# Performance work log

Hardware: AMD Instinct MI355X
Metric: run time of the kernel (lower is better)

The kernel has to match this reference:

```python
import jax, jax.numpy as jnp
import numpy as np

B, H, W = 2, 192, 192
DIM, HEADS, WS = 192, 6, 16
NT, RD, GS = 128, 20, 128
MLP_HID, TD_F, KS = 384, 48, 5
EPS = 1e-5


def _layernorm(x, g, b):
    m = jnp.mean(x, -1, keepdims=True)
    v = jnp.var(x, -1, keepdims=True)
    return (x - m) / jnp.sqrt(v + EPS) * g + b


def _l2n(x):
    return x / jnp.maximum(jnp.linalg.norm(x, axis=-1, keepdims=True), 1e-12)


def _rpi(ws):
    coords = np.stack(np.meshgrid(np.arange(ws), np.arange(ws), indexing='ij'))
    cf = coords.reshape(2, -1)
    rc = (cf[:, :, None] - cf[:, None, :]).transpose(1, 2, 0)
    rc[..., 0] += ws - 1
    rc[..., 1] += ws - 1
    rc[..., 0] *= 2 * ws - 1
    return rc.sum(-1)  # (ws*ws, ws*ws)


RPI = _rpi(WS)


def _win_attn(qkv, rpb, proj_w, h, w):
    # plain W-MSA (shift_size = 0 -> no mask, no roll)
    b, n, c3 = qkv.shape
    c = c3 // 3
    hd = c // HEADS
    nw = WS * WS
    xw = qkv.reshape(b, h // WS, WS, w // WS, WS, c3).transpose(0, 1, 3, 2, 4, 5).reshape(-1, nw, c3)
    bw = xw.shape[0]
    q, k, v = xw.reshape(bw, nw, 3, HEADS, hd).transpose(2, 0, 3, 1, 4)
    attn = (q * hd ** -0.5) @ k.swapaxes(-2, -1)  # (bw, heads, nw, nw)
    bias = rpb[RPI.reshape(-1)].reshape(nw, nw, HEADS).transpose(2, 0, 1)
    attn = jax.nn.softmax(attn + bias[None])
    out = (attn @ v).swapaxes(1, 2).reshape(bw, nw, c) @ proj_w
    out = out.reshape(b, h // WS, w // WS, WS, WS, c).transpose(0, 1, 3, 2, 4, 5).reshape(b, n, c)
    return out


def _atd_ca(x, td, wq, wk, wv, scale_p):
    q = _l2n(x @ wq)   # (b,n,rd)
    k = _l2n(td @ wk)  # (b,m,rd)
    v = td @ wv        # (b,m,c)
    scale = 1.0 + jnp.clip(scale_p, 0.0, 3.0) * np.log(NT)
    attn = jax.nn.softmax((q @ k.swapaxes(-2, -1)) * scale)  # (b,n,m)
    return attn @ v, attn


def _ac_msa(qkv, tk_id, proj_w):
    b, n, c3 = qkv.shape
    c = c3 // 3
    gs = min(n, GS)
    ng = (n + gs - 1) // gs
    pad = ng * gs - n
    idx = jnp.argsort(tk_id, axis=-1)          # sort tokens by category id
    inv = jnp.argsort(idx, axis=-1)            # inverse permutation
    sq = jnp.take_along_axis(qkv, idx[..., None], axis=1)
    if pad > 0:
        sq = jnp.concatenate([sq, sq[:, n - pad:n][:, ::-1]], axis=1)
    q, k, v = sq.reshape(b, ng, gs, 3, HEADS, c // HEADS).transpose(3, 0, 1, 4, 2, 5)
    attn = jax.nn.softmax((q @ k.swapaxes(-2, -1)) * (c // HEADS) ** -0.5)
    out = (attn @ v).transpose(0, 1, 3, 2, 4).reshape(b, ng * gs, c)[:, :n]
    out = jnp.take_along_axis(out, inv[..., None], axis=1)
    return out @ proj_w


def _convffn(x, x_td, w1, dw, w2, h, w):
    y = jnp.concatenate([jax.nn.gelu(x @ w1, approximate=False), x_td], axis=-1)
    b, n, ch = y.shape
    img = y.swapaxes(1, 2).reshape(b, ch, h, w)
    p = (KS - 1) // 2
    conv = jax.lax.conv_general_dilated(img, dw, (1, 1), [(p, p), (p, p)],
                                        dimension_numbers=('NCHW', 'OIHW', 'NCHW'),
                                        feature_group_count=ch)
    conv = jax.nn.gelu(conv, approximate=False).reshape(b, ch, n).swapaxes(1, 2)
    return (y + conv) @ w2


def setup_inputs():
    key = jax.random.key(0)
    ks = jax.random.split(key, 16)
    p = lambda k, s: jax.random.normal(k, s, jnp.float32) * 0.02
    return {
        'x': jax.random.normal(ks[0], (B, H * W, DIM), jnp.float32),
        'td': jax.random.normal(ks[1], (B, NT, DIM), jnp.float32),
        'norm1_g': jnp.ones((DIM,), jnp.float32), 'norm1_b': jnp.zeros((DIM,), jnp.float32),
        'norm2_g': jnp.ones((DIM,), jnp.float32), 'norm2_b': jnp.zeros((DIM,), jnp.float32),
        'wqkv': p(ks[2], (DIM, 3 * DIM)),
        'rpb': p(ks[3], ((2 * WS - 1) ** 2, HEADS)),
        'win_proj': p(ks[4], (DIM, DIM)),
        'atd_wq': p(ks[5], (DIM, RD)),
        'atd_wk': p(ks[6], (DIM, RD)),
        'atd_wv': p(ks[7], (DIM, DIM)),
        'atd_scale': jnp.ones((1,), jnp.float32),
        'aca_proj': p(ks[8], (DIM, DIM)),
        'fc_td_w': p(ks[9], (DIM, TD_F)),
        'ffn_w1': p(ks[10], (DIM, MLP_HID)),
        'ffn_dw': p(ks[11], (MLP_HID + TD_F, 1, KS, KS)),
        'ffn_w2': p(ks[12], (MLP_HID + TD_F, DIM)),
        'h': H, 'w': W,
    }


def reference(x, td, norm1_g, norm1_b, norm2_g, norm2_b, wqkv, rpb, win_proj,
              atd_wq, atd_wk, atd_wv, atd_scale, aca_proj, fc_td_w,
              ffn_w1, ffn_dw, ffn_w2, h, w):
    shortcut = x
    xn = _layernorm(x, norm1_g, norm1_b)
    qkv = xn @ wqkv  # (b, n, 3c)
    x_atd, sim = _atd_ca(xn, td, atd_wq, atd_wk, atd_wv, atd_scale)
    x_aca = _ac_msa(qkv, jnp.argmax(sim, axis=-1), aca_proj)
    x_win = _win_attn(qkv, rpb, win_proj, h, w)
    x = shortcut + x_win + x_atd + x_aca
    x_td = sim @ (td @ fc_td_w)  # (b, n, td_f): dictionary features routed by cross-attn weights
    x = x + _convffn(_layernorm(x, norm2_g, norm2_b), x_td, ffn_w1, ffn_dw, ffn_w2, h, w)
    return x
```

## Files before the change

kernel.cpp:

```cpp
#include <hip/hip_runtime.h>
#include <hip/hip_bf16.h>
#include <math.h>

#define NTOK 36864
#define NTOT 73728
#define CDIM 192
#define C3   576
#define NH   6
#define HD   32
#define RD   20
#define NTD  128
#define GSZ  128
#define NGRP 288
#define MLP  384
#define TDF  48
#define CH   432
#define RAWLD 384
#define TDO_LD 260

typedef __hip_bfloat16 bf16;
typedef __attribute__((ext_vector_type(8))) short short8;
typedef __attribute__((ext_vector_type(4))) float f32x4;

__device__ __forceinline__ float gelu_f(float x) {
    float u = x * (1.5957691216f + 0.0713548162f * x * x);
    return x / (1.0f + __expf(-u));
}

__device__ __forceinline__ unsigned short f32_to_bf16u(float f) {
    unsigned int u = __float_as_uint(f);
    u = (u + 0x7FFFu + ((u >> 16) & 1u)) >> 16;
    return (unsigned short)u;
}

__device__ __forceinline__ unsigned pack2bf(float a, float b) {
    return (__float_as_uint(a) >> 16) | (__float_as_uint(b) & 0xFFFF0000u);
}

__device__ __forceinline__ float bfbits2f(unsigned short u) {
    return __uint_as_float(((unsigned)u) << 16);
}

#define PACKW_TOT (192*576 + 192*192*2 + 192*384 + 432*192 + 192*16 + 192*TDO_LD)

__global__ void ln1_packw_kernel(
        const float* __restrict__ x, const float* __restrict__ g,
        const float* __restrict__ be, float* __restrict__ outf,
        bf16* __restrict__ outh,
        const float* __restrict__ wqkv, const float* __restrict__ wproj,
        const float* __restrict__ aproj, const float* __restrict__ w1,
        const float* __restrict__ w2,
        const float* __restrict__ awk, const float* __restrict__ awv,
        const float* __restrict__ fcw,
        bf16* __restrict__ wqkvT, bf16* __restrict__ projT,
        bf16* __restrict__ w1T, bf16* __restrict__ w2T,
        float* __restrict__ wcomb) {
    if (blockIdx.x < NTOT / 4) {
        long tok = (long)blockIdx.x * 4 + (threadIdx.x >> 6);
        int lane = threadIdx.x & 63;
        const float* row = x + tok * CDIM;
        float v0 = row[lane], v1 = row[lane + 64], v2 = row[lane + 128];
        float s  = v0 + v1 + v2;
        float ss = v0 * v0 + v1 * v1 + v2 * v2;
        #pragma unroll
        for (int o = 32; o > 0; o >>= 1) {
            s  += __shfl_down(s, o);
            ss += __shfl_down(ss, o);
        }
        s = __shfl(s, 0); ss = __shfl(ss, 0);
        float mean = s * (1.0f / 192.0f);
        float var  = ss * (1.0f / 192.0f) - mean * mean;
        float rstd = rsqrtf(var + 1e-5f);
        float r0 = (v0 - mean) * rstd * g[lane]       + be[lane];
        float r1 = (v1 - mean) * rstd * g[lane + 64]  + be[lane + 64];
        float r2 = (v2 - mean) * rstd * g[lane + 128] + be[lane + 128];
        float* orow = outf + tok * CDIM;
        orow[lane] = r0; orow[lane + 64] = r1; orow[lane + 128] = r2;
        bf16* hrow = outh + tok * CDIM;
        hrow[lane]       = __float2bfloat16(r0);
        hrow[lane + 64]  = __float2bfloat16(r1);
        hrow[lane + 128] = __float2bfloat16(r2);
        return;
    }
    int i = (blockIdx.x - NTOT / 4) * 256 + threadIdx.x;
    const int S0 = 192 * 576, S1 = 192 * 192, S2 = 192 * 192, S3 = 192 * 384,
              S4 = 432 * 192, S5 = 192 * 16, S6 = 192 * TDO_LD;
    if (i < S0) { int k = i / 576, n = i % 576; wqkvT[(long)n * 192 + k] = __float2bfloat16(wqkv[i]); return; }
    i -= S0;
    if (i < S1) { int k = i / 192, n = i % 192; projT[(long)n * 384 + k] = __float2bfloat16(wproj[i]); return; }
    i -= S1;
    if (i < S2) { int k = i / 192, n = i % 192; projT[(long)n * 384 + 192 + k] = __float2bfloat16(aproj[i]); return; }
    i -= S2;
    if (i < S3) { int k = i / 384, n = i % 384; w1T[(long)n * 192 + k] = __float2bfloat16(w1[i]); return; }
    i -= S3;
    if (i < S4) { int k = i / 192, n = i % 192; w2T[(long)n * 448 + k] = __float2bfloat16(w2[i]); return; }
    i -= S4;
    if (i < S5) { int n = i / 16, k = i % 16; w2T[(long)n * 448 + 432 + k] = __float2bfloat16(0.0f); return; }
    i -= S5;
    if (i < S6) {
        int k = i / TDO_LD, n = i % TDO_LD;
        float v;
        if (n < RD)            v = awk[k * RD + n];
        else if (n < RD + 192) v = awv[k * 192 + (n - RD)];
        else                   v = fcw[k * TDF + (n - RD - 192)];
        wcomb[(long)k * TDO_LD + n] = v;
    }
}

__global__ void ln2_kernel(const float* __restrict__ x, const float* __restrict__ g,
                           const float* __restrict__ be, bf16* __restrict__ outh) {
    long tok = (long)blockIdx.x * 4 + (threadIdx.x >> 6);
    int lane = threadIdx.x & 63;
    const float* row = x + tok * CDIM;
    float v0 = row[lane], v1 = row[lane + 64], v2 = row[lane + 128];
    float s  = v0 + v1 + v2;
    float ss = v0 * v0 + v1 * v1 + v2 * v2;
    #pragma unroll
    for (int o = 32; o > 0; o >>= 1) {
        s  += __shfl_down(s, o);
        ss += __shfl_down(ss, o);
    }
    s = __shfl(s, 0); ss = __shfl(ss, 0);
    float mean = s * (1.0f / 192.0f);
    float var  = ss * (1.0f / 192.0f) - mean * mean;
    float rstd = rsqrtf(var + 1e-5f);
    float r0 = (v0 - mean) * rstd * g[lane]       + be[lane];
    float r1 = (v1 - mean) * rstd * g[lane + 64]  + be[lane + 64];
    float r2 = (v2 - mean) * rstd * g[lane + 128] + be[lane + 128];
    bf16* hrow = outh + tok * CDIM;
    hrow[lane]       = __float2bfloat16(r0);
    hrow[lane + 64]  = __float2bfloat16(r1);
    hrow[lane + 128] = __float2bfloat16(r2);
}

#define LDT 72
template<int ACC, int GELU, int BF16OUT, int CHUNK8, int ADDX, int PL8OUT = 0>
__global__ void __launch_bounds__(256) gemm_bt(
        const bf16* __restrict__ A, const bf16* __restrict__ Bt,
        void* __restrict__ Cv, const float* __restrict__ Xadd,
        int M, int N, int K, int lda, int ldbt, int ldc,
        long sA, long sB, long sC) {
    long bz = blockIdx.z;
    A  += bz * sA;
    Bt += bz * sB;
    if (BF16OUT) Cv = (void*)((bf16*)Cv + bz * sC);
    else         Cv = (void*)((float*)Cv + bz * sC);
    if (ADDX) Xadd += bz * sC;

    __shared__ short As[128 * LDT];
    __shared__ short Bs[64 * LDT];
    int tid  = threadIdx.x;
    int lane = tid & 63;
    int w    = tid >> 6;
    int wr = w >> 1, wc = w & 1;
    int row0 = blockIdx.y * 128, col0 = blockIdx.x * 64;
    int fr = lane & 15, fq = lane >> 4;
    f32x4 acc[4][2];
    #pragma unroll
    for (int m = 0; m < 4; ++m)
        #pragma unroll
        for (int n = 0; n < 2; ++n) acc[m][n] = (f32x4)(0.0f);

    int sa_row = tid >> 3;
    int sa_kc  = (tid & 7) * 8;
    int sb_col = tid & 63;
    int sb_kb  = (tid >> 6) * 16;
    bool cok = (col0 + sb_col) < N;

    for (int k0 = 0; k0 < K; k0 += 64) {
        __syncthreads();
        int kk = k0 + sa_kc;
        #pragma unroll
        for (int p = 0; p < 4; ++p) {
            int r = sa_row + p * 32;
            short8 v = (short8)(0);
            if (kk + 8 <= K) {
                const bf16* src;
                if (CHUNK8)
                    src = A + ((long)(kk >> 3) * NTOT + row0 + r) * 8;
                else
                    src = A + (long)(row0 + r) * lda + kk;
                v = *(const short8*)src;
            } else if (!CHUNK8 && kk < K) {
                #pragma unroll
                for (int i = 0; i < 8; ++i)
                    v[i] = (kk + i < K) ? *(const short*)&A[(long)(row0 + r) * lda + kk + i]
                                        : (short)0;
            }
            *(short8*)&As[r * LDT + sa_kc] = v;
        }
        {
            short8 v0 = (short8)(0), v1 = (short8)(0);
            if (cok) {
                const bf16* src = Bt + (long)(col0 + sb_col) * ldbt + k0 + sb_kb;
                v0 = *(const short8*)src;
                v1 = *(const short8*)(src + 8);
            }
            *(short8*)&Bs[sb_col * LDT + sb_kb]     = v0;
            *(short8*)&Bs[sb_col * LDT + sb_kb + 8] = v1;
        }
        __syncthreads();
        short8 af[4][2], bf_[2][2];
        #pragma unroll
        for (int m = 0; m < 4; ++m) {
            int r = wr * 64 + m * 16 + fr;
            af[m][0] = *(const short8*)&As[r * LDT + fq * 8];
            af[m][1] = *(const short8*)&As[r * LDT + 32 + fq * 8];
        }
        #pragma unroll
        for (int n = 0; n < 2; ++n) {
            int c = wc * 32 + n * 16 + fr;
            bf_[n][0] = *(const short8*)&Bs[c * LDT + fq * 8];
            bf_[n][1] = *(const short8*)&Bs[c * LDT + 32 + fq * 8];
        }
        #pragma unroll
        for (int m = 0; m < 4; ++m)
            #pragma unroll
            for (int n = 0; n < 2; ++n) {
                acc[m][n] = __builtin_amdgcn_mfma_f32_16x16x32_bf16(
                                af[m][0], bf_[n][0], acc[m][n], 0, 0, 0);
                acc[m][n] = __builtin_amdgcn_mfma_f32_16x16x32_bf16(
                                af[m][1], bf_[n][1], acc[m][n], 0, 0, 0);
            }
    }
    #pragma unroll
    for (int m = 0; m < 4; ++m) {
        #pragma unroll
        for (int n = 0; n < 2; ++n) {
            int gc = col0 + wc * 32 + n * 16 + fr;
            if (gc >= N) continue;
            #pragma unroll
            for (int r = 0; r < 4; ++r) {
                int gr = row0 + wr * 64 + m * 16 + fq * 4 + r;
                float vv = acc[m][n][r];
                if (GELU) vv = gelu_f(vv);
                if (BF16OUT) {
                    long o;
                    if (PL8OUT) o = ((long)(gc >> 3) * NTOT + gr) * 8 + (gc & 7);
                    else        o = (long)gr * ldc + gc;
                    ((bf16*)Cv)[o] = __float2bfloat16(vv);
                } else {
                    long o = (long)gr * ldc + gc;
                    float* Cc = (float*)Cv;
                    if (ADDX) Cc[o] = Xadd[o] + vv;
                    else if (ACC) Cc[o] += vv;
                    else Cc[o] = vv;
                }
            }
        }
    }
}

template<int ACC, int GELU, int TDPACK>
__global__ void __launch_bounds__(256) gemm_kernel(
        const float* __restrict__ A, const float* __restrict__ B,
        float* __restrict__ Cc, int M, int N, int K, int lda, int ldb, int ldc,
        bf16* __restrict__ vtdT, bf16* __restrict__ tdfT) {
    __shared__ float As[16][68];
    __shared__ float Bs[16][68];
    int tid = threadIdx.x;
    int tr = tid >> 4, tc = tid & 15;
    int row0 = blockIdx.y * 64, col0 = blockIdx.x * 64;
    float acc[4][4] = {};
    int lm = tid >> 4;
    int lk = tid & 15;
    int bk = tid >> 6;
    int bn = tid & 63;
    for (int k0 = 0; k0 < K; k0 += 16) {
        #pragma unroll
        for (int i = 0; i < 4; ++i) {
            int m = lm + i * 16;
            int gr = row0 + m;
            As[lk][m] = (gr < M) ? A[(long)gr * lda + (k0 + lk)] : 0.0f;
        }
        #pragma unroll
        for (int i = 0; i < 4; ++i) {
            int kk = bk + i * 4;
            int gc = col0 + bn;
            Bs[kk][bn] = (gc < N) ? B[(long)(k0 + kk) * ldb + gc] : 0.0f;
        }
        __syncthreads();
        #pragma unroll
        for (int kk = 0; kk < 16; ++kk) {
            float4 av = *(const float4*)&As[kk][tr * 4];
            float4 bv = *(const float4*)&Bs[kk][tc * 4];
            float a[4] = {av.x, av.y, av.z, av.w};
            float b[4] = {bv.x, bv.y, bv.z, bv.w};
            #pragma unroll
            for (int i = 0; i < 4; ++i)
                #pragma unroll
                for (int j = 0; j < 4; ++j)
                    acc[i][j] = fmaf(a[i], b[j], acc[i][j]);
        }
        __syncthreads();
    }
    #pragma unroll
    for (int i = 0; i < 4; ++i) {
        int gr = row0 + tr * 4 + i;
        if (gr >= M) continue;
        #pragma unroll
        for (int j = 0; j < 4; ++j) {
            int gc = col0 + tc * 4 + j;
            if (gc >= N) continue;
            float v = acc[i][j];
            if (GELU) v = gelu_f(v);
            long o = (long)gr * ldc + gc;
            if (ACC) Cc[o] += v; else Cc[o] = v;
            if (TDPACK && gc >= RD) {
                bf16 hv = __float2bfloat16(v);
                int bb = gr >> 7;
                int kk2 = gr & (NTD - 1);
                if (gc < RD + CDIM)
                    vtdT[(long)bb * CDIM * NTD + (long)(gc - RD) * NTD + kk2] = hv;
                else
                    tdfT[(long)bb * TDF * NTD + (long)(gc - RD - CDIM) * NTD + kk2] = hv;
            }
        }
    }
}

__global__ void __launch_bounds__(256) qn_kernel(
        const float* __restrict__ xn, const float* __restrict__ awq,
        float* __restrict__ qn) {
    __shared__ float aw[192 * RD];
    __shared__ float xs[256 * 33];
    int tid = threadIdx.x;
    long tok0 = (long)blockIdx.x * 256;
    for (int e = tid; e < 192 * RD; e += 256) aw[e] = awq[e];
    float acc[RD];
    #pragma unroll
    for (int j = 0; j < RD; ++j) acc[j] = 0.0f;
    for (int kc = 0; kc < 192; kc += 32) {
        __syncthreads();
        for (int e = tid; e < 256 * 32; e += 256) {
            int tk = e >> 5, kk = e & 31;
            xs[tk * 33 + kk] = xn[(tok0 + tk) * CDIM + kc + kk];
        }
        __syncthreads();
        #pragma unroll 8
        for (int kk = 0; kk < 32; ++kk) {
            float v = xs[tid * 33 + kk];
            const float* ar = &aw[(kc + kk) * RD];
            #pragma unroll
            for (int j = 0; j < RD; ++j) acc[j] = fmaf(v, ar[j], acc[j]);
        }
    }
    float ss = 0.0f;
    #pragma unroll
    for (int j = 0; j < RD; ++j) ss += acc[j] * acc[j];
    float inv = 1.0f / fmaxf(sqrtf(ss), 1e-12f);
    float* orow = qn + (tok0 + tid) * RD;
    #pragma unroll
    for (int j = 0; j < RD; ++j) orow[j] = acc[j] * inv;
}

__global__ void __launch_bounds__(256) sim_kernel(
        const float* __restrict__ qn, const float* __restrict__ kn,
        const float* __restrict__ scale_p, bf16* __restrict__ sim,
        int* __restrict__ tkid) {
    int lane = threadIdx.x & 63;
    long tok = (long)blockIdx.x * 4 + (threadIdx.x >> 6);
    int b = (tok >= NTOK) ? 1 : 0;
    float q[RD];
    const float* qrow = qn + tok * RD;
    #pragma unroll
    for (int r = 0; r < RD; ++r) q[r] = qrow[r];
    const float* k0 = kn + ((long)b * NTD + lane) * TDO_LD;
    const float* k1 = k0 + (long)64 * TDO_LD;
    float k0v[RD], k1v[RD];
    #pragma unroll
    for (int r = 0; r < RD; ++r) { k0v[r] = k0[r]; k1v[r] = k1[r]; }
    float ss0 = 0.0f, ss1 = 0.0f;
    #pragma unroll
    for (int r = 0; r < RD; ++r) {
        ss0 += k0v[r] * k0v[r];
        ss1 += k1v[r] * k1v[r];
    }
    float inv0 = 1.0f / fmaxf(sqrtf(ss0), 1e-12f);
    float inv1 = 1.0f / fmaxf(sqrtf(ss1), 1e-12f);
    float s0 = 0.0f, s1 = 0.0f;
    #pragma unroll
    for (int r = 0; r < RD; ++r) {
        s0 = fmaf(q[r], k0v[r] * inv0, s0);
        s1 = fmaf(q[r], k1v[r] * inv1, s1);
    }
    float scl = 1.0f + fminf(fmaxf(scale_p[0], 0.0f), 3.0f) * logf(128.0f);
    s0 *= scl; s1 *= scl;
    float m; int mi;
    if (s0 >= s1) { m = s0; mi = lane; } else { m = s1; mi = lane + 64; }
    #pragma unroll
    for (int o = 1; o < 64; o <<= 1) {
        float om = __shfl_xor(m, o);
        int   oi = __shfl_xor(mi, o);
        if (om > m || (om == m && oi < mi)) { m = om; mi = oi; }
    }
    float p0 = __expf(s0 - m), p1 = __expf(s1 - m);
    float t = p0 + p1;
    #pragma unroll
    for (int o = 1; o < 64; o <<= 1) t += __shfl_xor(t, o);
    float inv = 1.0f / t;
    bf16* srow = sim + tok * NTD;
    srow[lane]      = __float2bfloat16(p0 * inv);
    srow[lane + 64] = __float2bfloat16(p1 * inv);
    if (lane == 0) tkid[tok] = mi;
}

__global__ void hist_kernel(const int* __restrict__ tkid, int* __restrict__ hist) {
    int tile = blockIdx.x;
    int tid = threadIdx.x;
    __shared__ int h[NTD];
    h[tid] = 0;
    __syncthreads();
    atomicAdd(&h[tkid[tile * GSZ + tid]], 1);
    __syncthreads();
    hist[tile * NTD + tid] = h[tid];
}

__global__ void __launch_bounds__(64) scan1_kernel(int* __restrict__ hist,
                                                   int* __restrict__ tot) {
    int bc = blockIdx.x;
    int b = bc >> 7, c = bc & (NTD - 1);
    int lane = threadIdx.x;
    if (lane < 32) {
        int base = (b * NGRP + lane * 9) * NTD + c;
        int v[9];
        int s = 0;
        #pragma unroll
        for (int k = 0; k < 9; ++k) { v[k] = hist[base + k * NTD]; s += v[k]; }
        int run = s;
        #pragma unroll
        for (int o = 1; o < 32; o <<= 1) {
            int t = __shfl_up(run, o);
            if (lane >= o) run += t;
        }
        if (lane == 31) tot[bc] = run;
        int acc = run - s;
        #pragma unroll
        for (int k = 0; k < 9; ++k) { hist[base + k * NTD] = acc; acc += v[k]; }
    }
}

__global__ void __launch_bounds__(128) scatter_kernel(const int* __restrict__ tkid,
                                                      const int* __restrict__ hist,
                                                      const int* __restrict__ tot,
                                                      int* __restrict__ idxs) {
    int tile = blockIdx.x;
    int b = tile / NGRP;
    int gl = tile % NGRP;
    int tid = threadIdx.x;
    __shared__ int cats[GSZ];
    __shared__ int basec[NTD];
    __shared__ int wsum[2];
    {
        int lane = tid & 63, wv = tid >> 6;
        int s = tot[b * NTD + tid];
        int run = s;
        #pragma unroll
        for (int o = 1; o < 64; o <<= 1) {
            int t = __shfl_up(run, o);
            if (lane >= o) run += t;
        }
        if (lane == 63) wsum[wv] = run;
        __syncthreads();
        int add = (wv == 1) ? wsum[0] : 0;
        basec[tid] = run - s + add;
    }
    int cat = tkid[tile * GSZ + tid];
    cats[tid] = cat;
    __syncthreads();
    int rank = 0;
    for (int j = 0; j < tid; ++j) rank += (cats[j] == cat) ? 1 : 0;
    int pos = hist[tile * NTD + cat] + basec[cat] + rank;
    idxs[b * NTOK + pos] = gl * GSZ + tid;
}

#define VLDW 264
#define VLDA 136


__global__ void __launch_bounds__(256) win_mfma(
        const bf16* __restrict__ qkv, const float* __restrict__ rpb,
        bf16* __restrict__ raw) {
    int t2  = blockIdx.x;
    int h   = t2 % NH;
    int wid = t2 / NH;
    int b = wid / 144;
    int wrem = wid % 144;
    int wy = wrem / 12, wx = wrem % 12;
    long base_tok = (long)b * NTOK;

    __shared__ short Kt[256 * 40];
    __shared__ short Vt[32 * VLDW];
    __shared__ float rb[961];

    int tid = threadIdx.x;
    int lane = tid & 63;
    int wv = tid >> 6;
    int fr = lane & 15, fq = lane >> 4;
    const float scl = 0.17677669529663687f;

    for (int i = tid; i < 961; i += 256) rb[i] = rpb[i * NH + h];

    short8 qf[4];
    #pragma unroll
    for (int m = 0; m < 4; ++m) {
        int q = wv * 64 + m * 16 + fr;
        long nq = base_tok + (long)(wy * 16 + (q >> 4)) * 192 + (wx * 16 + (q & 15));
        qf[m] = *(const short8*)(qkv + nq * C3 + h * HD + fq * 8);
    }

    {
        int s_ = tid >> 2, ch = tid & 3;
        #pragma unroll
        for (int t = 0; t < 4; ++t) {
            int p = t * 64 + s_;
            long nk = base_tok + (long)(wy * 16 + (p >> 4)) * 192 + (wx * 16 + (p & 15));
            const bf16* kb = qkv + nk * C3 + CDIM + h * HD + ch * 8;
            *(short8*)&Kt[p * 40 + ch * 8] = *(const short8*)kb;
            short8 vv = *(const short8*)(kb + CDIM);
            #pragma unroll
            for (int i = 0; i < 8; ++i)
                Vt[(ch * 8 + i) * VLDW + p] = vv[i];
        }
    }
    __syncthreads();

    f32x4 acc[4][2];
    float lst[4];
    #pragma unroll
    for (int m = 0; m < 4; ++m) {
        acc[m][0] = (f32x4)(0.0f); acc[m][1] = (f32x4)(0.0f);
        lst[m] = 0.0f;
    }

    for (int t = 0; t < 4; ++t) {
        short8 ak[4], av[2][2];
        #pragma unroll
        for (int c = 0; c < 4; ++c)
            ak[c] = *(const short8*)&Kt[(t * 64 + c * 16 + fr) * 40 + fq * 8];
        #pragma unroll
        for (int n = 0; n < 2; ++n)
            #pragma unroll
            for (int ks = 0; ks < 2; ++ks)
                av[n][ks] = *(const short8*)&Vt[(n * 16 + fr) * VLDW + t * 64 + ks * 32 + fq * 8];

        #pragma unroll
        for (int m = 0; m < 4; ++m) {
            int q = wv * 64 + m * 16 + fr;
            int iy = q >> 4, ix = q & 15;
            int bxb = ix + 15 - 4 * fq;
            float s[4][4];
            #pragma unroll
            for (int c = 0; c < 4; ++c) {
                f32x4 s4 = (f32x4)(0.0f);
                s4 = __builtin_amdgcn_mfma_f32_16x16x32_bf16(ak[c], qf[m], s4, 0, 0, 0);
                const float* rbp = &rb[(iy + 15 - (t * 4 + c)) * 31 + bxb];
                #pragma unroll
                for (int r = 0; r < 4; ++r)
                    s[c][r] = s4[r] * scl + rbp[-r];
            }
            float ps = 0.0f;
            #pragma unroll
            for (int c = 0; c < 4; ++c)
                #pragma unroll
                for (int r = 0; r < 4; ++r) {
                    float p = __expf(s[c][r]);
                    s[c][r] = p;
                    ps += p;
                }
            ps += __shfl_xor(ps, 16);
            ps += __shfl_xor(ps, 32);
            lst[m] += ps;
            unsigned pk[4][2];
            #pragma unroll
            for (int c = 0; c < 4; ++c) {
                pk[c][0] = pack2bf(s[c][0], s[c][1]);
                pk[c][1] = pack2bf(s[c][2], s[c][3]);
            }
            #pragma unroll
            for (int ks = 0; ks < 2; ++ks) {
                unsigned u[4];
                #pragma unroll
                for (int jj = 0; jj < 4; ++jj) {
                    int src = fr + 16 * (2 * (fq & 1) + (jj >> 1));
                    unsigned lo = (unsigned)__shfl((int)pk[2 * ks][jj & 1], src);
                    unsigned hi = (unsigned)__shfl((int)pk[2 * ks + 1][jj & 1], src);
                    u[jj] = (fq & 2) ? hi : lo;
                }
                short8 pb;
                #pragma unroll
                for (int jj = 0; jj < 4; ++jj) {
                    pb[2 * jj]     = (short)(u[jj] & 0xFFFF);
                    pb[2 * jj + 1] = (short)(u[jj] >> 16);
                }
                #pragma unroll
                for (int n = 0; n < 2; ++n)
                    acc[m][n] = __builtin_amdgcn_mfma_f32_16x16x32_bf16(
                                    av[n][ks], pb, acc[m][n], 0, 0, 0);
            }
        }
    }
    #pragma unroll
    for (int m = 0; m < 4; ++m) {
        int q = wv * 64 + m * 16 + fr;
        long nq = base_tok + (long)(wy * 16 + (q >> 4)) * 192 + (wx * 16 + (q & 15));
        float inv = 1.0f / lst[m];
        #pragma unroll
        for (int n = 0; n < 2; ++n) {
            uint2 wv2;
            wv2.x = pack2bf(acc[m][n][0] * inv, acc[m][n][1] * inv);
            wv2.y = pack2bf(acc[m][n][2] * inv, acc[m][n][3] * inv);
            *(uint2*)(raw + nq * RAWLD + h * HD + n * 16 + 4 * fq) = wv2;
        }
    }
}

__global__ void __launch_bounds__(128) aca_mfma(
        const bf16* __restrict__ qkv, const int* __restrict__ idxs,
        bf16* __restrict__ raw) {
    int t2   = blockIdx.x;
    int h    = t2 % NH;
    int grp  = t2 / NH;
    int b = grp / NGRP;
    int g = grp % NGRP;
    long btok = (long)b * NTOK;

    __shared__ short Kt[128 * 40];
    __shared__ short Vt[32 * VLDA];
    __shared__ int   sidx[GSZ];

    int tid = threadIdx.x;
    int lane = tid & 63;
    int half = tid >> 6;
    int fr = lane & 15, fq = lane >> 4;
    const float scl = 0.17677669529663687f;

    sidx[tid] = idxs[btok + g * GSZ + tid];
    __syncthreads();

    short8 qf[4];
    #pragma unroll
    for (int m = 0; m < 4; ++m) {
        long n = btok + sidx[half * 64 + m * 16 + fr];
        qf[m] = *(const short8*)(qkv + n * C3 + h * HD + fq * 8);
    }

    {
        int s_ = tid >> 1, hf = tid & 1;
        int d0 = hf * 16;
        #pragma unroll
        for (int t = 0; t < 2; ++t) {
            int p = t * 64 + s_;
            long n = btok + sidx[p];
            const bf16* kb = qkv + n * C3 + CDIM + h * HD + d0;
            *(short8*)&Kt[p * 40 + d0]     = *(const short8*)kb;
            *(short8*)&Kt[p * 40 + d0 + 8] = *(const short8*)(kb + 8);
            short8 v0 = *(const short8*)(kb + CDIM);
            short8 v1 = *(const short8*)(kb + CDIM + 8);
            #pragma unroll
            for (int i = 0; i < 8; ++i) {
                Vt[(d0 + i) * VLDA + p]     = v0[i];
                Vt[(d0 + 8 + i) * VLDA + p] = v1[i];
            }
        }
    }
    __syncthreads();

    f32x4 acc[4][2];
    float lst[4];
    #pragma unroll
    for (int m = 0; m < 4; ++m) {
        acc[m][0] = (f32x4)(0.0f); acc[m][1] = (f32x4)(0.0f);
        lst[m] = 0.0f;
    }

    for (int t = 0; t < 2; ++t) {
        short8 ak[4], av[2][2];
        #pragma unroll
        for (int c = 0; c < 4; ++c)
            ak[c] = *(const short8*)&Kt[(t * 64 + c * 16 + fr) * 40 + fq * 8];
        #pragma unroll
        for (int n = 0; n < 2; ++n)
            #pragma unroll
            for (int ks = 0; ks < 2; ++ks)
                av[n][ks] = *(const short8*)&Vt[(n * 16 + fr) * VLDA + t * 64 + ks * 32 + fq * 8];

        #pragma unroll
        for (int m = 0; m < 4; ++m) {
            float s[4][4];
            #pragma unroll
            for (int c = 0; c < 4; ++c) {
                f32x4 s4 = (f32x4)(0.0f);
                s4 = __builtin_amdgcn_mfma_f32_16x16x32_bf16(ak[c], qf[m], s4, 0, 0, 0);
                #pragma unroll
                for (int r = 0; r < 4; ++r) s[c][r] = s4[r] * scl;
            }
            float ps = 0.0f;
            #pragma unroll
            for (int c = 0; c < 4; ++c)
                #pragma unroll
                for (int r = 0; r < 4; ++r) {
                    float p = __expf(s[c][r]);
                    s[c][r] = p;
                    ps += p;
                }
            ps += __shfl_xor(ps, 16);
            ps += __shfl_xor(ps, 32);
            lst[m] += ps;
            unsigned pk[4][2];
            #pragma unroll
            for (int c = 0; c < 4; ++c) {
                pk[c][0] = pack2bf(s[c][0], s[c][1]);
                pk[c][1] = pack2bf(s[c][2], s[c][3]);
            }
            #pragma unroll
            for (int ks = 0; ks < 2; ++ks) {
                unsigned u[4];
                #pragma unroll
                for (int jj = 0; jj < 4; ++jj) {
                    int src = fr + 16 * (2 * (fq & 1) + (jj >> 1));
                    unsigned lo = (unsigned)__shfl((int)pk[2 * ks][jj & 1], src);
                    unsigned hi = (unsigned)__shfl((int)pk[2 * ks + 1][jj & 1], src);
                    u[jj] = (fq & 2) ? hi : lo;
                }
                short8 pb;
                #pragma unroll
                for (int jj = 0; jj < 4; ++jj) {
                    pb[2 * jj]     = (short)(u[jj] & 0xFFFF);
                    pb[2 * jj + 1] = (short)(u[jj] >> 16);
                }
                #pragma unroll
                for (int n = 0; n < 2; ++n)
                    acc[m][n] = __builtin_amdgcn_mfma_f32_16x16x32_bf16(
                                    av[n][ks], pb, acc[m][n], 0, 0, 0);
            }
        }
    }
    #pragma unroll
    for (int m = 0; m < 4; ++m) {
        long n = btok + sidx[half * 64 + m * 16 + fr];
        float inv = 1.0f / lst[m];
        #pragma unroll
        for (int nn = 0; nn < 2; ++nn) {
            uint2 wv2;
            wv2.x = pack2bf(acc[m][nn][0] * inv, acc[m][nn][1] * inv);
            wv2.y = pack2bf(acc[m][nn][2] * inv, acc[m][nn][3] * inv);
            *(uint2*)(raw + n * RAWLD + CDIM + h * HD + nn * 16 + 4 * fq) = wv2;
        }
    }
}

#define CPS 1296
__global__ void __launch_bounds__(256) conv_kernel(
        const bf16* __restrict__ y, const float* __restrict__ dw,
        bf16* __restrict__ zc) {
    int bid = blockIdx.x;
    int ck   = bid % 54;
    int tile = (bid / 54) % 36;
    int b    = bid / (54 * 36);
    int ty = tile / 6, tx = tile % 6;
    int c0 = ck * 8;
    __shared__ float ys[8 * CPS];
    __shared__ float wt[8 * 25];
    int tid = threadIdx.x;
    const bf16* ypl = y + ((long)ck * NTOT + (long)b * NTOK) * 8;
    for (int p = tid; p < 1296; p += 256) {
        int ly = p / 36, lx = p - ly * 36;
        int gy = ty * 32 + ly - 2, gx = tx * 32 + lx - 2;
        float f[8];
        if (gy >= 0 && gy < 192 && gx >= 0 && gx < 192) {
            short8 hv = *(const short8*)(ypl + (long)(gy * 192 + gx) * 8);
            #pragma unroll
            for (int i = 0; i < 8; ++i) f[i] = bfbits2f((unsigned short)hv[i]);
        } else {
            #pragma unroll
            for (int i = 0; i < 8; ++i) f[i] = 0.0f;
        }
        #pragma unroll
        for (int i = 0; i < 8; ++i) ys[i * CPS + p] = f[i];
    }
    for (int e = tid; e < 200; e += 256) wt[e] = dw[c0 * 25 + e];
    __syncthreads();
    int col = tid & 31, r4 = tid >> 5;
    int py0 = r4 * 4;
    long tok0 = (long)b * NTOK + (long)(ty * 32 + py0) * 192 + tx * 32 + col;
    unsigned hh[4][4];
    for (int c = 0; c < 8; ++c) {
        const float* yc = &ys[c * CPS];
        float w[25];
        #pragma unroll
        for (int t = 0; t < 25; ++t) w[t] = wt[c * 25 + t];
        float a[4] = {0.0f, 0.0f, 0.0f, 0.0f};
        #pragma unroll
        for (int dy2 = 0; dy2 < 8; ++dy2) {
            float rv[5];
            #pragma unroll
            for (int dx = 0; dx < 5; ++dx)
                rv[dx] = yc[(py0 + dy2) * 36 + col + dx];
            #pragma unroll
            for (int i = 0; i < 4; ++i) {
                int dy = dy2 - i;
                if (dy >= 0 && dy < 5) {
                    #pragma unroll
                    for (int dx = 0; dx < 5; ++dx)
                        a[i] = fmaf(rv[dx], w[dy * 5 + dx], a[i]);
                }
            }
        }
        #pragma unroll
        for (int i = 0; i < 4; ++i) {
            float center = yc[(py0 + i + 2) * 36 + col + 2];
            unsigned short hsh = f32_to_bf16u(center + gelu_f(a[i]));
            if (c & 1) hh[i][c >> 1] |= ((unsigned)hsh) << 16;
            else       hh[i][c >> 1] = (unsigned)hsh;
        }
    }
    #pragma unroll
    for (int i = 0; i < 4; ++i) {
        long tok = tok0 + (long)i * 192;
        *(uint4*)(zc + ((long)ck * NTOT + tok) * 8) =
            make_uint4(hh[i][0], hh[i][1], hh[i][2], hh[i][3]);
    }
}

extern "C" void kernel_launch(void* const* d_in, const int* in_sizes, int n_in,
                              void* d_out, int out_size, void* d_ws, size_t ws_size,
                              hipStream_t stream) {
    (void)in_sizes; (void)n_in; (void)out_size; (void)ws_size;
    const float* x     = (const float*)d_in[0];
    const float* td    = (const float*)d_in[1];
    const float* n1g   = (const float*)d_in[2];
    const float* n1b   = (const float*)d_in[3];
    const float* n2g   = (const float*)d_in[4];
    const float* n2b   = (const float*)d_in[5];
    const float* wqkv  = (const float*)d_in[6];
    const float* rpb   = (const float*)d_in[7];
    const float* wproj = (const float*)d_in[8];
    const float* awq   = (const float*)d_in[9];
    const float* awk   = (const float*)d_in[10];
    const float* awv   = (const float*)d_in[11];
    const float* ascl  = (const float*)d_in[12];
    const float* aproj = (const float*)d_in[13];
    const float* fcw   = (const float*)d_in[14];
    const float* w1    = (const float*)d_in[15];
    const float* dw    = (const float*)d_in[16];
    const float* w2    = (const float*)d_in[17];
    float* out = (float*)d_out;

    char* ws = (char*)d_ws;
    size_t off = 0;
    auto alloc = [&](size_t bytes) -> char* {
        char* p = ws + off;
        off += (bytes + 255) & ~(size_t)255;
        return p;
    };
    bf16*  qkv  = (bf16*)alloc((size_t)NTOT * C3 * 2);
    float* xn   = (float*)alloc((size_t)NTOT * CDIM * 4);
    bf16*  xnh  = (bf16*)alloc((size_t)NTOT * CDIM * 2);
    float* qn   = (float*)alloc((size_t)NTOT * RD * 4);
    bf16*  simb = (bf16*)alloc((size_t)NTOT * NTD * 2);
    float* tdo  = (float*)alloc((size_t)2 * NTD * TDO_LD * 4);
    float* wcomb= (float*)alloc((size_t)192 * TDO_LD * 4);
    bf16*  vtdT = (bf16*)alloc((size_t)2 * CDIM * NTD * 2);
    bf16*  tdfT = (bf16*)alloc((size_t)2 * TDF * NTD * 2);
    bf16*  wqkvT= (bf16*)alloc((size_t)C3 * CDIM * 2);
    bf16*  projT= (bf16*)alloc((size_t)CDIM * 384 * 2);
    bf16*  w1T  = (bf16*)alloc((size_t)MLP * CDIM * 2);
    bf16*  w2T  = (bf16*)alloc((size_t)CDIM * 448 * 2);
    int*   tkid = (int*)alloc((size_t)NTOT * 4);
    int*   idxs = (int*)alloc((size_t)NTOT * 4);
    int*   hist = (int*)alloc((size_t)576 * NTD * 4);
    int*   tot  = (int*)alloc((size_t)2 * NTD * 4);
    bf16*  y    = qkv;
    bf16*  raw  = (bf16*)xn;
    bf16*  zc   = (bf16*)xn;

    ln1_packw_kernel<<<NTOT / 4 + (PACKW_TOT + 255) / 256, 256, 0, stream>>>(
        x, n1g, n1b, xn, xnh,
        wqkv, wproj, aproj, w1, w2, awk, awv, fcw,
        wqkvT, projT, w1T, w2T, wcomb);

    gemm_bt<0,0,1,0,0><<<dim3(9, 576), 256, 0, stream>>>(
        xnh, wqkvT, qkv, nullptr, NTOT, C3, CDIM, CDIM, CDIM, C3, 0, 0, 0);

    qn_kernel<<<NTOT / 256, 256, 0, stream>>>(xn, awq, qn);

    gemm_kernel<0,0,1><<<dim3(5, 4), 256, 0, stream>>>(
        td, wcomb, tdo, 2 * NTD, TDO_LD, CDIM, CDIM, TDO_LD, TDO_LD, vtdT, tdfT);

    sim_kernel<<<NTOT / 4, 256, 0, stream>>>(qn, tdo, ascl, simb, tkid);

    gemm_bt<0,0,0,0,1><<<dim3(3, 288, 2), 256, 0, stream>>>(
        simb, vtdT, out, x, NTOK, CDIM, NTD, NTD, NTD, CDIM,
        (long)NTOK * NTD, (long)CDIM * NTD, (long)NTOK * CDIM);

    hist_kernel<<<576, 128, 0, stream>>>(tkid, hist);
    scan1_kernel<<<2 * NTD, 64, 0, stream>>>(hist, tot);
    scatter_kernel<<<576, 128, 0, stream>>>(tkid, hist, tot, idxs);

    win_mfma<<<288 * NH, 256, 0, stream>>>(qkv, rpb, raw);
    aca_mfma<<<576 * NH, 128, 0, stream>>>(qkv, idxs, raw);
    gemm_bt<1,0,0,0,0><<<dim3(3, 576), 256, 0, stream>>>(
        raw, projT, out, nullptr, NTOT, CDIM, 384, RAWLD, 384, CDIM, 0, 0, 0);

    gemm_bt<0,0,1,0,0,1><<<dim3(1, 288, 2), 256, 0, stream>>>(
        simb, tdfT, y + (long)48 * NTOT * 8, nullptr, NTOK, TDF, NTD, NTD, NTD, 0,
        (long)NTOK * NTD, (long)TDF * NTD, (long)NTOK * 8);

    ln2_kernel<<<NTOT / 4, 256, 0, stream>>>(out, n2g, n2b, xnh);

    gemm_bt<0,1,1,0,0,1><<<dim3(6, 576), 256, 0, stream>>>(
        xnh, w1T, y, nullptr, NTOT, MLP, CDIM, CDIM, CDIM, 0, 0, 0, 0);

    conv_kernel<<<2 * 36 * 54, 256, 0, stream>>>(y, dw, zc);
    gemm_bt<1,0,0,1,0><<<dim3(3, 576), 256, 0, stream>>>(
        zc, w2T, out, nullptr, NTOT, CDIM, CH, 0, 448, CDIM, 0, 0, 0);
}
```

Measured before the change: 663.6 us.

## Fold histogram into sim kernel and merge window and category attention launches

Drops the separate histogram kernel: the LN1/weight-pack kernel now zeroes the histogram buffer, and sim_kernel adds each token's argmax straight into the per-tile histogram with a global atomic. The window-attention and category-attention kernels are merged into one launch that picks its role from the block index, with two 128-thread category subgroups packed per 256-thread block over shared memory. This removes two kernel launches and lets both attention types run at the same time, at the cost of global atomic contention in sim_kernel and a larger shared-memory footprint for the category blocks. The category path still has __syncthreads across both subgroups, which is fine as long as the control flow is uniform.

```diff
diff --git a/kernel.cpp b/kernel.cpp
--- a/kernel.cpp
+++ b/kernel.cpp
@@ -42,6 +42,7 @@
 }
 
 #define PACKW_TOT (192*576 + 192*192*2 + 192*384 + 432*192 + 192*16 + 192*TDO_LD)
+#define HISTZ_TOT (576 * NTD)
 
 __global__ void ln1_packw_kernel(
         const float* __restrict__ x, const float* __restrict__ g,
@@ -54,7 +55,7 @@
         const float* __restrict__ fcw,
         bf16* __restrict__ wqkvT, bf16* __restrict__ projT,
         bf16* __restrict__ w1T, bf16* __restrict__ w2T,
-        float* __restrict__ wcomb) {
+        float* __restrict__ wcomb, int* __restrict__ hist) {
     if (blockIdx.x < NTOT / 4) {
         long tok = (long)blockIdx.x * 4 + (threadIdx.x >> 6);
         int lane = threadIdx.x & 63;
@@ -84,7 +85,7 @@
     }
     int i = (blockIdx.x - NTOT / 4) * 256 + threadIdx.x;
     const int S0 = 192 * 576, S1 = 192 * 192, S2 = 192 * 192, S3 = 192 * 384,
-              S4 = 432 * 192, S5 = 192 * 16, S6 = 192 * TDO_LD;
+              S4 = 432 * 192, S5 = 192 * 16, S6 = 192 * TDO_LD, S7 = HISTZ_TOT;
     if (i < S0) { int k = i / 576, n = i % 576; wqkvT[(long)n * 192 + k] = __float2bfloat16(wqkv[i]); return; }
     i -= S0;
     if (i < S1) { int k = i / 192, n = i % 192; projT[(long)n * 384 + k] = __float2bfloat16(wproj[i]); return; }
@@ -104,7 +105,10 @@
         else if (n < RD + 192) v = awv[k * 192 + (n - RD)];
         else                   v = fcw[k * TDF + (n - RD - 192)];
         wcomb[(long)k * TDO_LD + n] = v;
-    }
+        return;
+    }
+    i -= S6;
+    if (i < S7) hist[i] = 0;
 }
 
 __global__ void ln2_kernel(const float* __restrict__ x, const float* __restrict__ g,
@@ -357,7 +361,7 @@
 __global__ void __launch_bounds__(256) sim_kernel(
         const float* __restrict__ qn, const float* __restrict__ kn,
         const float* __restrict__ scale_p, bf16* __restrict__ sim,
-        int* __restrict__ tkid) {
+        int* __restrict__ tkid, int* __restrict__ hist) {
     int lane = threadIdx.x & 63;
     long tok = (long)blockIdx.x * 4 + (threadIdx.x >> 6);
     int b = (tok >= NTOK) ? 1 : 0;
@@ -402,18 +406,10 @@
     bf16* srow = sim + tok * NTD;
     srow[lane]      = __float2bfloat16(p0 * inv);
     srow[lane + 64] = __float2bfloat16(p1 * inv);
-    if (lane == 0) tkid[tok] = mi;
-}
-
-__global__ void hist_kernel(const int* __restrict__ tkid, int* __restrict__ hist) {
-    int tile = blockIdx.x;
-    int tid = threadIdx.x;
-    __shared__ int h[NTD];
-    h[tid] = 0;
-    __syncthreads();
-    atomicAdd(&h[tkid[tile * GSZ + tid]], 1);
-    __syncthreads();
-    hist[tile * NTD + tid] = h[tid];
+    if (lane == 0) {
+        tkid[tok] = mi;
+        atomicAdd(&hist[(tok >> 7) * NTD + mi], 1);
+    }
 }
 
 __global__ void __launch_bounds__(64) scan1_kernel(int* __restrict__ hist,
@@ -477,165 +473,165 @@
 #define VLDW 264
 #define VLDA 136
 
-
-__global__ void __launch_bounds__(256) win_mfma(
+#define WIN_BLOCKS (288 * NH)
+__global__ void __launch_bounds__(256) attn_mfma(
         const bf16* __restrict__ qkv, const float* __restrict__ rpb,
-        bf16* __restrict__ raw) {
-    int t2  = blockIdx.x;
-    int h   = t2 % NH;
-    int wid = t2 / NH;
-    int b = wid / 144;
-    int wrem = wid % 144;
-    int wy = wrem / 12, wx = wrem % 12;
-    long base_tok = (long)b * NTOK;
-
-    __shared__ short Kt[256 * 40];
-    __shared__ short Vt[32 * VLDW];
-    __shared__ float rb[961];
-
+        const int* __restrict__ idxs, bf16* __restrict__ raw) {
+    __shared__ __align__(16) char smem[41280];
     int tid = threadIdx.x;
-    int lane = tid & 63;
-    int wv = tid >> 6;
-    int fr = lane & 15, fq = lane >> 4;
-    const float scl = 0.17677669529663687f;
-
-    for (int i = tid; i < 961; i += 256) rb[i] = rpb[i * NH + h];
-
-    short8 qf[4];
-    #pragma unroll
-    for (int m = 0; m < 4; ++m) {
-        int q = wv * 64 + m * 16 + fr;
-        long nq = base_tok + (long)(wy * 16 + (q >> 4)) * 192 + (wx * 16 + (q & 15));
-        qf[m] = *(const short8*)(qkv + nq * C3 + h * HD + fq * 8);
-    }
-
-    {
-        int s_ = tid >> 2, ch = tid & 3;
-        #pragma unroll
-        for (int t = 0; t < 4; ++t) {
-            int p = t * 64 + s_;
-            long nk = base_tok + (long)(wy * 16 + (p >> 4)) * 192 + (wx * 16 + (p & 15));
-            const bf16* kb = qkv + nk * C3 + CDIM + h * HD + ch * 8;
-            *(short8*)&Kt[p * 40 + ch * 8] = *(const short8*)kb;
-            short8 vv = *(const short8*)(kb + CDIM);
-            #pragma unroll
-            for (int i = 0; i < 8; ++i)
-                Vt[(ch * 8 + i) * VLDW + p] = vv[i];
-        }
-    }
-    __syncthreads();
-
-    f32x4 acc[4][2];
-    float lst[4];
-    #pragma unroll
-    for (int m = 0; m < 4; ++m) {
-        acc[m][0] = (f32x4)(0.0f); acc[m][1] = (f32x4)(0.0f);
-        lst[m] = 0.0f;
-    }
-
-    for (int t = 0; t < 4; ++t) {
-        short8 ak[4], av[2][2];
-        #pragma unroll
-        for (int c = 0; c < 4; ++c)
-            ak[c] = *(const short8*)&Kt[(t * 64 + c * 16 + fr) * 40 + fq * 8];
-        #pragma unroll
-        for (int n = 0; n < 2; ++n)
-            #pragma unroll
-            for (int ks = 0; ks < 2; ++ks)
-                av[n][ks] = *(const short8*)&Vt[(n * 16 + fr) * VLDW + t * 64 + ks * 32 + fq * 8];
-
+
+    if (blockIdx.x < WIN_BLOCKS) {
+        short* Kt = (short*)smem;
+        short* Vt = (short*)(smem + 20480);
+        float* rb = (float*)(smem + 20480 + 16896);
+        int t2  = blockIdx.x;
+        int h   = t2 % NH;
+        int wid = t2 / NH;
+        int b = wid / 144;
+        int wrem = wid % 144;
+        int wy = wrem / 12, wx = wrem % 12;
+        long base_tok = (long)b * NTOK;
+
+        int lane = tid & 63;
+        int wv = tid >> 6;
+        int fr = lane & 15, fq = lane >> 4;
+        const float scl = 0.17677669529663687f;
+
+        for (int i = tid; i < 961; i += 256) rb[i] = rpb[i * NH + h];
+
+        short8 qf[4];
         #pragma unroll
         for (int m = 0; m < 4; ++m) {
             int q = wv * 64 + m * 16 + fr;
-            int iy = q >> 4, ix = q & 15;
-            int bxb = ix + 15 - 4 * fq;
-            float s[4][4];
-            #pragma unroll
-            for (int c = 0; c < 4; ++c) {
-                f32x4 s4 = (f32x4)(0.0f);
-                s4 = __builtin_amdgcn_mfma_f32_16x16x32_bf16(ak[c], qf[m], s4, 0, 0, 0);
-                const float* rbp = &rb[(iy + 15 - (t * 4 + c)) * 31 + bxb];
-                #pragma unroll
-                for (int r = 0; r < 4; ++r)
-                    s[c][r] = s4[r] * scl + rbp[-r];
-            }
-            float ps = 0.0f;
+            long nq = base_tok + (long)(wy * 16 + (q >> 4)) * 192 + (wx * 16 + (q & 15));
+            qf[m] = *(const short8*)(qkv + nq * C3 + h * HD + fq * 8);
+        }
+
+        {
+            int s_ = tid >> 2, ch = tid & 3;
+            #pragma unroll
+            for (int t = 0; t < 4; ++t) {
+                int p = t * 64 + s_;
+                long nk = base_tok + (long)(wy * 16 + (p >> 4)) * 192 + (wx * 16 + (p & 15));
+                const bf16* kb = qkv + nk * C3 + CDIM + h * HD + ch * 8;
+                *(short8*)&Kt[p * 40 + ch * 8] = *(const short8*)kb;
+                short8 vv = *(const short8*)(kb + CDIM);
+                #pragma unroll
+                for (int i = 0; i < 8; ++i)
+                    Vt[(ch * 8 + i) * VLDW + p] = vv[i];
+            }
+        }
+        __syncthreads();
+
+        f32x4 acc[4][2];
+        float lst[4];
+        #pragma unroll
+        for (int m = 0; m < 4; ++m) {
+            acc[m][0] = (f32x4)(0.0f); acc[m][1] = (f32x4)(0.0f);
+            lst[m] = 0.0f;
+        }
+
+        for (int t = 0; t < 4; ++t) {
+            short8 ak[4], av[2][2];
             #pragma unroll
             for (int c = 0; c < 4; ++c)
-                #pragma unroll
-                for (int r = 0; r < 4; ++r) {
-                    float p = __expf(s[c][r]);
-                    s[c][r] = p;
-                    ps += p;
+                ak[c] = *(const short8*)&Kt[(t * 64 + c * 16 + fr) * 40 + fq * 8];
+            #pragma unroll
+            for (int n = 0; n < 2; ++n)
+                #pragma unroll
+                for (int ks = 0; ks < 2; ++ks)
+                    av[n][ks] = *(const short8*)&Vt[(n * 16 + fr) * VLDW + t * 64 + ks * 32 + fq * 8];
+
+            #pragma unroll
+            for (int m = 0; m < 4; ++m) {
+                int q = wv * 64 + m * 16 + fr;
+                int iy = q >> 4, ix = q & 15;
+                int bxb = ix + 15 - 4 * fq;
+                float s[4][4];
+                #pragma unroll
+                for (int c = 0; c < 4; ++c) {
+                    f32x4 s4 = (f32x4)(0.0f);
+                    s4 = __builtin_amdgcn_mfma_f32_16x16x32_bf16(ak[c], qf[m], s4, 0, 0, 0);
+                    const float* rbp = &rb[(iy + 15 - (t * 4 + c)) * 31 + bxb];
+                    #pragma unroll
+                    for (int r = 0; r < 4; ++r)
+                        s[c][r] = s4[r] * scl + rbp[-r];
                 }
-            ps += __shfl_xor(ps, 16);
-            ps += __shfl_xor(ps, 32);
-            lst[m] += ps;
-            unsigned pk[4][2];
-            #pragma unroll
-            for (int c = 0; c < 4; ++c) {
-                pk[c][0] = pack2bf(s[c][0], s[c][1]);
-                pk[c][1] = pack2bf(s[c][2], s[c][3]);
-            }
-            #pragma unroll
-            for (int ks = 0; ks < 2; ++ks) {
-                unsigned u[4];
-                #pragma unroll
-                for (int jj = 0; jj < 4; ++jj) {
-                    int src = fr + 16 * (2 * (fq & 1) + (jj >> 1));
-                    unsigned lo = (unsigned)__shfl((int)pk[2 * ks][jj & 1], src);
-                    unsigned hi = (unsigned)__shfl((int)pk[2 * ks + 1][jj & 1], src);
-                    u[jj] = (fq & 2) ? hi : lo;
+                float ps = 0.0f;
+                #pragma unroll
+                for (int c = 0; c < 4; ++c)
+                    #pragma unroll
+                    for (int r = 0; r < 4; ++r) {
+                        float p = __expf(s[c][r]);
+                        s[c][r] = p;
+                        ps += p;
+                    }
+                ps += __shfl_xor(ps, 16);
+                ps += __shfl_xor(ps, 32);
+                lst[m] += ps;
+                unsigned pk[4][2];
+                #pragma unroll
+                for (int c = 0; c < 4; ++c) {
+                    pk[c][0] = pack2bf(s[c][0], s[c][1]);
+                    pk[c][1] = pack2bf(s[c][2], s[c][3]);
                 }
-                short8 pb;
-                #pragma unroll
-                for (int jj = 0; jj < 4; ++jj) {
-                    pb[2 * jj]     = (short)(u[jj] & 0xFFFF);
-                    pb[2 * jj + 1] = (short)(u[jj] >> 16);
+                #pragma unroll
+                for (int ks = 0; ks < 2; ++ks) {
+                    unsigned u[4];
+                    #pragma unroll
+                    for (int jj = 0; jj < 4; ++jj) {
+                        int src = fr + 16 * (2 * (fq & 1) + (jj >> 1));
+                        unsigned lo = (unsigned)__shfl((int)pk[2 * ks][jj & 1], src);
+                        unsigned hi = (unsigned)__shfl((int)pk[2 * ks + 1][jj & 1], src);
+                        u[jj] = (fq & 2) ? hi : lo;
+                    }
+                    short8 pb;
+                    #pragma unroll
+                    for (int jj = 0; jj < 4; ++jj) {
+                        pb[2 * jj]     = (short)(u[jj] & 0xFFFF);
+                        pb[2 * jj + 1] = (short)(u[jj] >> 16);
+                    }
+                    #pragma unroll
+                    for (int n = 0; n < 2; ++n)
+                        acc[m][n] = __builtin_amdgcn_mfma_f32_16x16x32_bf16(
+                                        av[n][ks], pb, acc[m][n], 0, 0, 0);
                 }
-                #pragma unroll
-                for (int n = 0; n < 2; ++n)
-                    acc[m][n] = __builtin_amdgcn_mfma_f32_16x16x32_bf16(
-                                    av[n][ks], pb, acc[m][n], 0, 0, 0);
-            }
-        }
-    }
-    #pragma unroll
-    for (int m = 0; m < 4; ++m) {
-        int q = wv * 64 + m * 16 + fr;
-        long nq = base_tok + (long)(wy * 16 + (q >> 4)) * 192 + (wx * 16 + (q & 15));
-        float inv = 1.0f / lst[m];
-        #pragma unroll
-        for (int n = 0; n < 2; ++n) {
-            uint2 wv2;
-            wv2.x = pack2bf(acc[m][n][0] * inv, acc[m][n][1] * inv);
-            wv2.y = pack2bf(acc[m][n][2] * inv, acc[m][n][3] * inv);
-            *(uint2*)(raw + nq * RAWLD + h * HD + n * 16 + 4 * fq) = wv2;
-        }
-    }
-}
-
-__global__ void __launch_bounds__(128) aca_mfma(
-        const bf16* __restrict__ qkv, const int* __restrict__ idxs,
-        bf16* __restrict__ raw) {
-    int t2   = blockIdx.x;
+            }
+        }
+        #pragma unroll
+        for (int m = 0; m < 4; ++m) {
+            int q = wv * 64 + m * 16 + fr;
+            long nq = base_tok + (long)(wy * 16 + (q >> 4)) * 192 + (wx * 16 + (q & 15));
+            float inv = 1.0f / lst[m];
+            #pragma unroll
+            for (int n = 0; n < 2; ++n) {
+                uint2 wv2;
+                wv2.x = pack2bf(acc[m][n][0] * inv, acc[m][n][1] * inv);
+                wv2.y = pack2bf(acc[m][n][2] * inv, acc[m][n][3] * inv);
+                *(uint2*)(raw + nq * RAWLD + h * HD + n * 16 + 4 * fq) = wv2;
+            }
+        }
+        return;
+    }
+
+    int sub  = tid >> 7;
+    int tidl = tid & 127;
+    int t2   = (blockIdx.x - WIN_BLOCKS) * 2 + sub;
+    short* Kt = (short*)(smem + sub * 19456);
+    short* Vt = (short*)(smem + sub * 19456 + 10240);
+    int* sidx = (int*)  (smem + sub * 19456 + 10240 + 8704);
     int h    = t2 % NH;
     int grp  = t2 / NH;
     int b = grp / NGRP;
     int g = grp % NGRP;
     long btok = (long)b * NTOK;
 
-    __shared__ short Kt[128 * 40];
-    __shared__ short Vt[32 * VLDA];
-    __shared__ int   sidx[GSZ];
-
-    int tid = threadIdx.x;
-    int lane = tid & 63;
-    int half = tid >> 6;
+    int lane = tidl & 63;
+    int half = tidl >> 6;
     int fr = lane & 15, fq = lane >> 4;
     const float scl = 0.17677669529663687f;
 
-    sidx[tid] = idxs[btok + g * GSZ + tid];
+    sidx[tidl] = idxs[btok + g * GSZ + tidl];
     __syncthreads();
 
     short8 qf[4];
@@ -646,7 +642,7 @@
     }
 
     {
-        int s_ = tid >> 1, hf = tid & 1;
+        int s_ = tidl >> 1, hf = tidl & 1;
         int d0 = hf * 16;
         #pragma unroll
         for (int t = 0; t < 2; ++t) {
@@ -875,10 +871,10 @@
     bf16*  raw  = (bf16*)xn;
     bf16*  zc   = (bf16*)xn;
 
-    ln1_packw_kernel<<<NTOT / 4 + (PACKW_TOT + 255) / 256, 256, 0, stream>>>(
+    ln1_packw_kernel<<<NTOT / 4 + (PACKW_TOT + HISTZ_TOT + 255) / 256, 256, 0, stream>>>(
         x, n1g, n1b, xn, xnh,
         wqkv, wproj, aproj, w1, w2, awk, awv, fcw,
-        wqkvT, projT, w1T, w2T, wcomb);
+        wqkvT, projT, w1T, w2T, wcomb, hist);
 
     gemm_bt<0,0,1,0,0><<<dim3(9, 576), 256, 0, stream>>>(
         xnh, wqkvT, qkv, nullptr, NTOT, C3, CDIM, CDIM, CDIM, C3, 0, 0, 0);
@@ -888,18 +884,16 @@
     gemm_kernel<0,0,1><<<dim3(5, 4), 256, 0, stream>>>(
         td, wcomb, tdo, 2 * NTD, TDO_LD, CDIM, CDIM, TDO_LD, TDO_LD, vtdT, tdfT);
 
-    sim_kernel<<<NTOT / 4, 256, 0, stream>>>(qn, tdo, ascl, simb, tkid);
+    sim_kernel<<<NTOT / 4, 256, 0, stream>>>(qn, tdo, ascl, simb, tkid, hist);
 
     gemm_bt<0,0,0,0,1><<<dim3(3, 288, 2), 256, 0, stream>>>(
         simb, vtdT, out, x, NTOK, CDIM, NTD, NTD, NTD, CDIM,
         (long)NTOK * NTD, (long)CDIM * NTD, (long)NTOK * CDIM);
 
-    hist_kernel<<<576, 128, 0, stream>>>(tkid, hist);
     scan1_kernel<<<2 * NTD, 64, 0, stream>>>(hist, tot);
     scatter_kernel<<<576, 128, 0, stream>>>(tkid, hist, tot, idxs);
 
-    win_mfma<<<288 * NH, 256, 0, stream>>>(qkv, rpb, raw);
-    aca_mfma<<<576 * NH, 128, 0, stream>>>(qkv, idxs, raw);
+    attn_mfma<<<WIN_BLOCKS + (576 * NH) / 2, 256, 0, stream>>>(qkv, rpb, idxs, raw);
     gemm_bt<1,0,0,0,0><<<dim3(3, 576), 256, 0, stream>>>(
         raw, projT, out, nullptr, NTOT, CDIM, 384, RAWLD, 384, CDIM, 0, 0, 0);
 
```

Result: no change. 656.0 us (median of 2 runs) (-1.1%).
